# Optimization experiments

Measured on AMD Instinct MI355X. Metric: run time of the kernel, lower is better.

## Reference

```python
import jax, jax.numpy as jnp
import numpy as np
from jax import lax

EPS_LN = 1e-5
EPS_NORM = 1e-12
NUM_HEADS = 8
KV_HEADS = 2
REP = NUM_HEADS // KV_HEADS


def _layernorm_c(x, w, b):
    # WithBias LayerNorm over channel dim; x: [b,c,h,w]
    mu = x.mean(axis=1, keepdims=True)
    var = ((x - mu) ** 2).mean(axis=1, keepdims=True)
    return (x - mu) / jnp.sqrt(var + EPS_LN) * w[None, :, None, None] + b[None, :, None, None]


def _conv1x1(x, w):
    # x: [b,c,h,w], w: [o,c]
    return jnp.einsum('bchw,oc->bohw', x, w)


def _dwconv3x3(x, w):
    # depthwise 3x3, SAME padding; w: [C,1,3,3]
    C = x.shape[1]
    return lax.conv_general_dilated(
        x, w, window_strides=(1, 1), padding='SAME',
        dimension_numbers=('NCHW', 'OIHW', 'NCHW'), feature_group_count=C)


def _l2norm(x):
    # normalize over last axis (torch F.normalize semantics)
    n = jnp.sqrt(jnp.sum(x * x, axis=-1, keepdims=True))
    return x / jnp.maximum(n, EPS_NORM)


def setup_inputs() -> dict:
    key = jax.random.key(0)
    ks = jax.random.split(key, 8)
    b, dim, h, w = 4, 192, 256, 256
    kv_ch = 2 * dim // REP  # 96
    return {
        'x': jax.random.normal(ks[0], (b, dim, h, w), jnp.float32),
        'ln_w': jnp.ones((dim,), jnp.float32),
        'ln_b': jnp.zeros((dim,), jnp.float32),
        'q_w': jax.random.normal(ks[1], (dim, dim), jnp.float32) * 0.02,
        'q_dw': jax.random.normal(ks[2], (dim, 1, 3, 3), jnp.float32) * 0.1,
        'kv_w': jax.random.normal(ks[3], (kv_ch, dim), jnp.float32) * 0.02,
        'kv_dw': jax.random.normal(ks[4], (kv_ch, 1, 3, 3), jnp.float32) * 0.1,
        'proj_w': jax.random.normal(ks[5], (dim, dim), jnp.float32) * 0.02,
        'temperature': jnp.ones((NUM_HEADS, 1, 1), jnp.float32),
    }


def reference(x, ln_w, ln_b, q_w, q_dw, kv_w, kv_dw, proj_w, temperature):
    b, c, h, w = x.shape
    xn = _layernorm_c(x, ln_w, ln_b)
    q = _dwconv3x3(_conv1x1(xn, q_w), q_dw)            # [b, c, h, w]
    kv = _dwconv3x3(_conv1x1(xn, kv_w), kv_dw)         # [b, 2c/rep, h, w]
    k, v = jnp.split(kv, 2, axis=1)
    hw = h * w
    ch = c // NUM_HEADS
    q = q.reshape(b, NUM_HEADS, ch, hw)
    k = k.reshape(b, KV_HEADS, ch, hw)
    v = v.reshape(b, KV_HEADS, ch, hw)
    k = jnp.repeat(k, REP, axis=1)                     # repeat_kv
    v = jnp.repeat(v, REP, axis=1)
    q = _l2norm(q)
    k = _l2norm(k)
    attn = jnp.einsum('bhcn,bhdn->bhcd', q, k) * temperature[None]
    attn = jax.nn.softmax(attn, axis=-1)
    out = jnp.einsum('bhcd,bhdn->bhcn', attn, v)
    out = out.reshape(b, c, h, w)
    return _conv1x1(out, proj_w)
```

## Files before the change

kernel.cpp:

```cpp
#include <hip/hip_runtime.h>
#include <hip/hip_bf16.h>
#include <stdint.h>

#define HW    65536
#define NB    4
#define CIN   192
#define OYC   288
#define BSTR  200
#define EPS2  264

__device__ __forceinline__ float bflo(unsigned u){ return __uint_as_float(u << 16); }
__device__ __forceinline__ float bfhi(unsigned u){ return __uint_as_float(u & 0xffff0000u); }
__device__ __forceinline__ float bf2f(__hip_bfloat16 v){ return __bfloat162float(v); }
__device__ __forceinline__ unsigned short f2bfbits(float f){
  __hip_bfloat16 h = __float2bfloat16(f); return *(unsigned short*)&h;
}

__device__ __forceinline__ void unpack8(uint4 u, float* f) {
  f[0]=bflo(u.x); f[1]=bfhi(u.x); f[2]=bflo(u.y); f[3]=bfhi(u.y);
  f[4]=bflo(u.z); f[5]=bfhi(u.z); f[6]=bflo(u.w); f[7]=bfhi(u.w);
}

union BF8 { uint4 u; __hip_bfloat16 h[8]; };

typedef __attribute__((ext_vector_type(8))) short short8;
typedef __attribute__((ext_vector_type(4))) float floatx4;

__global__ void k_prep(const float* __restrict__ qw, const float* __restrict__ kvw,
                       const float* __restrict__ lnw, const float* __restrict__ lnb,
                       __hip_bfloat16* __restrict__ AF, float* __restrict__ bias,
                       float* __restrict__ Ssum) {
  int blk = blockIdx.x, t = threadIdx.x;
  if (blk < 32) {
    for (int i = blk * 256 + t; i < OYC * CIN; i += 32 * 256) {
      int o = i / CIN, c = i % CIN;
      float w = (o < 192) ? qw[o * 192 + c] : kvw[(o - 192) * 192 + c];
      float val = w * lnw[c];
      int ot = o >> 4, lo = o & 15;
      int ks = c >> 5, cr = c & 31, q = cr >> 3, j = cr & 7;
      int dst = (((ot * 6 + ks) * 64) + q * 16 + lo) * 8 + j;
      AF[dst] = __float2bfloat16(val);
    }
  } else {
    for (int o = t; o < OYC; o += 256) {
      float s = 0.f, s2 = 0.f;
      for (int c = 0; c < CIN; ++c) {
        float w = (o < 192) ? qw[o * 192 + c] : kvw[(o - 192) * 192 + c];
        s += w * lnb[c];
        s2 += bf2f(__float2bfloat16(w * lnw[c]));
      }
      bias[o] = s;
      Ssum[o] = s2;
    }
  }
}

__global__ __launch_bounds__(512, 2) void k_conv1r(const float* __restrict__ x,
                                                   const __hip_bfloat16* __restrict__ AF,
                                                   const float* __restrict__ bias,
                                                   const float* __restrict__ Ssum,
                                                   __hip_bfloat16* __restrict__ y) {
  __shared__ __align__(16) __hip_bfloat16 Bl[256 * BSTR];
  __shared__ float part_s[8][256];
  __shared__ float part_q[8][256];
  __shared__ float murs[256][2];
  __shared__ float biasl[OYC];
  __shared__ float Sl[OYC];

  int bid = blockIdx.x;
  int b = bid >> 8;
  int r = bid & 255;
  int tid = threadIdx.x;
  int w = tid >> 6, l = tid & 63;

  for (int i = tid; i < OYC; i += 512) { biasl[i] = bias[i]; Sl[i] = Ssum[i]; }

  {
    const float* xb = x + (size_t)(b * CIN + w * 24) * HW + r * 256 + l * 4;
    float s[4] = {0.f, 0.f, 0.f, 0.f}, q2[4] = {0.f, 0.f, 0.f, 0.f};
    unsigned pk[4][12];
#pragma unroll
    for (int c = 0; c < 24; ++c) {
      float4 v4 = *(const float4*)(xb + (size_t)c * HW);
      float vv[4] = {v4.x, v4.y, v4.z, v4.w};
#pragma unroll
      for (int i = 0; i < 4; ++i) {
        s[i] += vv[i]; q2[i] += vv[i] * vv[i];
        unsigned bits = f2bfbits(vv[i]);
        if ((c & 1) == 0) pk[i][c >> 1] = bits;
        else              pk[i][c >> 1] |= bits << 16;
      }
    }
#pragma unroll
    for (int i = 0; i < 4; ++i) {
      int px = l * 4 + i;
#pragma unroll
      for (int j = 0; j < 3; ++j) {
        uint4 u = make_uint4(pk[i][j*4], pk[i][j*4+1], pk[i][j*4+2], pk[i][j*4+3]);
        *(uint4*)&Bl[px * BSTR + w * 24 + j * 8] = u;
      }
    }
    *(float4*)&part_s[w][l * 4] = make_float4(s[0], s[1], s[2], s[3]);
    *(float4*)&part_q[w][l * 4] = make_float4(q2[0], q2[1], q2[2], q2[3]);
  }
  __syncthreads();

  int lane = tid & 63;
  int mh = w >> 2, nq = w & 3;
  int li = lane & 15, qd = lane >> 4;

  floatx4 acc[9][4];
#pragma unroll
  for (int t = 0; t < 9; ++t)
#pragma unroll
    for (int nt = 0; nt < 4; ++nt) acc[t][nt] = (floatx4){0.f, 0.f, 0.f, 0.f};

  const __hip_bfloat16* abase = AF + ((size_t)(mh * 9) * 6 * 64 + lane) * 8;
  short8 a0[9], a1[9];
#pragma unroll
  for (int t = 0; t < 9; ++t) a0[t] = *(const short8*)(abase + (size_t)(t * 6) * 512);

#pragma unroll
  for (int ks = 0; ks < 6; ++ks) {
    short8 bf[4];
#pragma unroll
    for (int nt = 0; nt < 4; ++nt) {
      int px = nq * 64 + nt * 16 + li;
      bf[nt] = *(const short8*)&Bl[px * BSTR + ks * 32 + qd * 8];
    }
    if (ks < 5) {
#pragma unroll
      for (int t = 0; t < 9; ++t) {
        short8 v = *(const short8*)(abase + (size_t)(t * 6 + ks + 1) * 512);
        if (ks & 1) a0[t] = v; else a1[t] = v;
      }
    }
#pragma unroll
    for (int t = 0; t < 9; ++t) {
      short8 af = (ks & 1) ? a1[t] : a0[t];
#pragma unroll
      for (int nt = 0; nt < 4; ++nt)
        acc[t][nt] = __builtin_amdgcn_mfma_f32_16x16x32_bf16(af, bf[nt], acc[t][nt], 0, 0, 0);
    }
  }

  if (tid < 256) {
    float s0 = 0.f, s1 = 0.f;
#pragma unroll
    for (int g = 0; g < 8; ++g) { s0 += part_s[g][tid]; s1 += part_q[g][tid]; }
    float m = s0 * (1.f / CIN);
    float var = s1 * (1.f / CIN) - m * m;
    murs[tid][0] = m;
    murs[tid][1] = rsqrtf(var + 1e-5f);
  }

  __hip_bfloat16* EP = Bl;
#pragma unroll
  for (int ph = 0; ph < 2; ++ph) {
    __syncthreads();
    if (mh == ph) {
#pragma unroll
      for (int t = 0; t < 9; ++t)
#pragma unroll
        for (int nt = 0; nt < 4; ++nt) {
          int px = nq * 64 + nt * 16 + li;
          float mu = murs[px][0], rs = murs[px][1];
#pragma unroll
          for (int rr = 0; rr < 4; ++rr) {
            int ol = t * 16 + qd * 4 + rr;
            float val = rs * (acc[t][nt][rr] - mu * Sl[ph * 144 + ol]) + biasl[ph * 144 + ol];
            EP[ol * EPS2 + px] = __float2bfloat16(val);
          }
        }
    }
    __syncthreads();
    for (int i = tid; i < 144 * 32; i += 512) {
      int row = i >> 5, seg = i & 31;
      uint4 u = *(const uint4*)&EP[row * EPS2 + seg * 8];
      *(uint4*)&y[(size_t)(b * OYC + ph * 144 + row) * HW + r * 256 + seg * 8] = u;
    }
  }
}

__global__ __launch_bounds__(256) void k_dwkv(const __hip_bfloat16* __restrict__ y,
                                              const float* __restrict__ kvdw,
                                              __hip_bfloat16* __restrict__ kbuf,
                                              __hip_bfloat16* __restrict__ vbuf,
                                              float* __restrict__ kss) {
  __shared__ __align__(16) __hip_bfloat16 stage[18 * 256];
  int bid = blockIdx.x;
  int hb = bid & 15;
  int ck = (bid >> 4) % 96;
  int b  = bid / (16 * 96);
  int tid = threadIdx.x;
  int h0 = hb * 16;

  const __hip_bfloat16* yp = y + (size_t)(b * OYC + 192 + ck) * HW;
  for (int i = tid; i < 18 * 32; i += 256) {
    int ry = i >> 5, seg = i & 31;
    int hh = h0 - 1 + ry;
    uint4 u = make_uint4(0u, 0u, 0u, 0u);
    if ((unsigned)hh < 256u) u = *(const uint4*)(yp + hh * 256 + seg * 8);
    *(uint4*)&stage[ry * 256 + seg * 8] = u;
  }
  __syncthreads();

  float w[9];
#pragma unroll
  for (int i = 0; i < 9; ++i) w[i] = kvdw[ck * 9 + i];

  int cg = tid & 31, rg = tid >> 5;
  int c0 = cg * 8;
  bool isk = (ck < 48);
  __hip_bfloat16* ob = (isk ? kbuf : vbuf) + (size_t)(b * 48 + (ck % 48)) * HW;
  float ssq = 0.f;
#pragma unroll
  for (int rr = 0; rr < 2; ++rr) {
    int orow = rg * 2 + rr;
    float o[8];
#pragma unroll
    for (int j = 0; j < 8; ++j) o[j] = 0.f;
#pragma unroll
    for (int ry = 0; ry < 3; ++ry) {
      const __hip_bfloat16* rb = &stage[(orow + ry) * 256];
      float v[8];
      unpack8(*(const uint4*)&rb[c0], v);
      float vl = (c0 > 0)       ? bf2f(rb[c0 - 1]) : 0.f;
      float vr = (c0 + 8 < 256) ? bf2f(rb[c0 + 8]) : 0.f;
      float wl = w[ry * 3], wm = w[ry * 3 + 1], wr = w[ry * 3 + 2];
      o[0] = fmaf(wl, vl, fmaf(wm, v[0], fmaf(wr, v[1], o[0])));
#pragma unroll
      for (int j = 1; j < 7; ++j)
        o[j] = fmaf(wl, v[j-1], fmaf(wm, v[j], fmaf(wr, v[j+1], o[j])));
      o[7] = fmaf(wl, v[6], fmaf(wm, v[7], fmaf(wr, vr, o[7])));
    }
    BF8 t;
#pragma unroll
    for (int j = 0; j < 8; ++j) {
      t.h[j] = __float2bfloat16(o[j]);
      if (isk) { float fv = bf2f(t.h[j]); ssq += fv * fv; }
    }
    *(uint4*)(ob + (size_t)(h0 + orow) * 256 + c0) = t.u;
  }
  if (isk) {
#pragma unroll
    for (int off = 32; off > 0; off >>= 1) ssq += __shfl_down(ssq, off);
    __shared__ float ws4[4];
    if ((tid & 63) == 0) ws4[tid >> 6] = ssq;
    __syncthreads();
    if (tid == 0) atomicAdd(&kss[b * 48 + ck], ws4[0] + ws4[1] + ws4[2] + ws4[3]);
  }
}

__global__ __launch_bounds__(256) void k_dwq(const __hip_bfloat16* __restrict__ y,
                                             const float* __restrict__ qdw,
                                             __hip_bfloat16* __restrict__ qfull,
                                             float* __restrict__ qss) {
  __shared__ __align__(16) __hip_bfloat16 stage[18 * 256];
  int bid = blockIdx.x;
  int hb = bid & 15;
  int c  = (bid >> 4) % 192;
  int b  = bid / (16 * 192);
  int tid = threadIdx.x;
  int h0 = hb * 16;

  const __hip_bfloat16* yp = y + (size_t)(b * OYC + c) * HW;
  for (int i = tid; i < 18 * 32; i += 256) {
    int ry = i >> 5, seg = i & 31;
    int hh = h0 - 1 + ry;
    uint4 u = make_uint4(0u, 0u, 0u, 0u);
    if ((unsigned)hh < 256u) u = *(const uint4*)(yp + hh * 256 + seg * 8);
    *(uint4*)&stage[ry * 256 + seg * 8] = u;
  }
  __syncthreads();

  float w[9];
#pragma unroll
  for (int i = 0; i < 9; ++i) w[i] = qdw[c * 9 + i];

  int cg = tid & 31, rg = tid >> 5;
  int c0 = cg * 8;
  __hip_bfloat16* ob = qfull + (size_t)(b * CIN + c) * HW;
  float ssq = 0.f;
#pragma unroll
  for (int rr = 0; rr < 2; ++rr) {
    int orow = rg * 2 + rr;
    float o[8];
#pragma unroll
    for (int j = 0; j < 8; ++j) o[j] = 0.f;
#pragma unroll
    for (int ry = 0; ry < 3; ++ry) {
      const __hip_bfloat16* rb = &stage[(orow + ry) * 256];
      float v[8];
      unpack8(*(const uint4*)&rb[c0], v);
      float vl = (c0 > 0)       ? bf2f(rb[c0 - 1]) : 0.f;
      float vr = (c0 + 8 < 256) ? bf2f(rb[c0 + 8]) : 0.f;
      float wl = w[ry * 3], wm = w[ry * 3 + 1], wr = w[ry * 3 + 2];
      o[0] = fmaf(wl, vl, fmaf(wm, v[0], fmaf(wr, v[1], o[0])));
#pragma unroll
      for (int j = 1; j < 7; ++j)
        o[j] = fmaf(wl, v[j-1], fmaf(wm, v[j], fmaf(wr, v[j+1], o[j])));
      o[7] = fmaf(wl, v[6], fmaf(wm, v[7], fmaf(wr, vr, o[7])));
    }
    BF8 t;
#pragma unroll
    for (int j = 0; j < 8; ++j) {
      t.h[j] = __float2bfloat16(o[j]);
      float fv = bf2f(t.h[j]); ssq += fv * fv;
    }
    *(uint4*)(ob + (size_t)(h0 + orow) * 256 + c0) = t.u;
  }
#pragma unroll
  for (int off = 32; off > 0; off >>= 1) ssq += __shfl_down(ssq, off);
  __shared__ float ws4[4];
  if ((tid & 63) == 0) ws4[tid >> 6] = ssq;
  __syncthreads();
  if (tid == 0) atomicAdd(&qss[b * 192 + c], ws4[0] + ws4[1] + ws4[2] + ws4[3]);
}

__global__ __launch_bounds__(256) void k_qk(const __hip_bfloat16* __restrict__ qfull,
                                            const __hip_bfloat16* __restrict__ kbuf,
                                            float* __restrict__ attn) {
  __shared__ __align__(16) __hip_bfloat16 ql[96 * 264];
  __shared__ __align__(16) __hip_bfloat16 kl[24 * 264];
  __shared__ float red[96 * 33];
  int bid = blockIdx.x;
  int ck  = bid & 63;
  int kvh = (bid >> 6) & 1;
  int b   = bid >> 7;
  int tid = threadIdx.x;
  int wave = tid >> 6, lane = tid & 63;
  int li = lane & 15, qd = lane >> 4;

  for (int i = tid; i < 96 * 33; i += 256) red[i] = 0.f;

  const __hip_bfloat16* qp = qfull + (size_t)(b * CIN + kvh * 96) * HW + ck * 1024;
  const __hip_bfloat16* kp = kbuf  + (size_t)(b * 48 + kvh * 24) * HW + ck * 1024;

  floatx4 acc[6][2];
#pragma unroll
  for (int mt = 0; mt < 6; ++mt) {
    acc[mt][0] = (floatx4){0.f, 0.f, 0.f, 0.f};
    acc[mt][1] = (floatx4){0.f, 0.f, 0.f, 0.f};
  }

  int kr1 = 16 + li; if (kr1 > 23) kr1 = 23;
  for (int sc = 0; sc < 4; ++sc) {
    __syncthreads();
    for (int i = tid; i < 96 * 32; i += 256) {
      int row = i >> 5, seg = i & 31;
      *(uint4*)&ql[row * 264 + seg * 8] = *(const uint4*)(qp + (size_t)row * HW + sc * 256 + seg * 8);
    }
    for (int i = tid; i < 24 * 32; i += 256) {
      int row = i >> 5, seg = i & 31;
      *(uint4*)&kl[row * 264 + seg * 8] = *(const uint4*)(kp + (size_t)row * HW + sc * 256 + seg * 8);
    }
    __syncthreads();
#pragma unroll
    for (int ks = 0; ks < 2; ++ks) {
      int off = wave * 64 + ks * 32 + qd * 8;
      short8 bk0 = *(const short8*)&kl[li  * 264 + off];
      short8 bk1 = *(const short8*)&kl[kr1 * 264 + off];
#pragma unroll
      for (int mt = 0; mt < 6; ++mt) {
        short8 aq = *(const short8*)&ql[(mt * 16 + li) * 264 + off];
        acc[mt][0] = __builtin_amdgcn_mfma_f32_16x16x32_bf16(aq, bk0, acc[mt][0], 0, 0, 0);
        acc[mt][1] = __builtin_amdgcn_mfma_f32_16x16x32_bf16(aq, bk1, acc[mt][1], 0, 0, 0);
      }
    }
  }

#pragma unroll
  for (int mt = 0; mt < 6; ++mt) {
#pragma unroll
    for (int nt = 0; nt < 2; ++nt) {
      int n = nt * 16 + li;
      if (n < 24) {
#pragma unroll
        for (int r = 0; r < 4; ++r) {
          int m = mt * 16 + qd * 4 + r;
          atomicAdd(&red[m * 33 + n], acc[mt][nt][r]);
        }
      }
    }
  }
  __syncthreads();

  for (int i = tid; i < 96 * 24; i += 256) {
    int m = i / 24, d = i % 24;
    int head = kvh * 4 + m / 24, cp = m % 24;
    atomicAdd(&attn[(((b * 8 + head) * 24) + cp) * 24 + d], red[m * 33 + d]);
  }
}

__global__ void k_attn_final(const float* __restrict__ attn, const float* __restrict__ qss,
                             const float* __restrict__ kss, const float* __restrict__ temp,
                             const float* __restrict__ projw, __hip_bfloat16* __restrict__ AB) {
  int b = blockIdx.x;
  int t = threadIdx.x;
  __shared__ float as_[96 * 25];
  float acc[48];
#pragma unroll
  for (int j = 0; j < 48; ++j) acc[j] = 0.f;
  for (int kvh = 0; kvh < 2; ++kvh) {
    __syncthreads();
    if (t < 96) {
      int row = kvh * 96 + t;
      int h = row / 24, cp = row % 24;
      float rq = 1.f / fmaxf(sqrtf(qss[b * 192 + row]), 1e-12f);
      float tp = temp[h];
      float lg[24]; float mx = -1e30f;
#pragma unroll
      for (int d = 0; d < 24; ++d) {
        float rk = 1.f / fmaxf(sqrtf(kss[b * 48 + kvh * 24 + d]), 1e-12f);
        float l = attn[(((b * 8 + h) * 24) + cp) * 24 + d] * rq * rk * tp;
        lg[d] = l; mx = fmaxf(mx, l);
      }
      float s = 0.f;
#pragma unroll
      for (int d = 0; d < 24; ++d) { lg[d] = __expf(lg[d] - mx); s += lg[d]; }
      float inv = 1.f / s;
#pragma unroll
      for (int d = 0; d < 24; ++d) as_[t * 25 + d] = lg[d] * inv;
    }
    __syncthreads();
    if (t < 192) {
      for (int cc = 0; cc < 96; ++cc) {
        float pw = projw[t * 192 + kvh * 96 + cc];
        const float* ar = &as_[cc * 25];
#pragma unroll
        for (int d = 0; d < 24; ++d) acc[kvh * 24 + d] = fmaf(pw, ar[d], acc[kvh * 24 + d]);
      }
    }
  }
  if (t < 192) {
    __hip_bfloat16* ABb = AB + (size_t)b * 18432;
    int mt = t >> 4, lb = t & 15;
#pragma unroll
    for (int g = 0; g < 12; ++g) {
      int kk0 = g * 8;
      int s = kk0 >> 5;
      int lane = lb + 16 * ((kk0 & 31) >> 3);
      BF8 u;
#pragma unroll
      for (int jj = 0; jj < 8; ++jj) {
        int kk = kk0 + jj;
        if (kk < 48) {
          u.h[jj] = __float2bfloat16(acc[kk]);
        } else {
          int j = kk - 48;
          float hv = bf2f(__float2bfloat16(acc[j]));
          u.h[jj] = __float2bfloat16(acc[j] - hv);
        }
      }
      *(uint4*)(ABb + (size_t)((mt * 3 + s) * 64 + lane) * 8) = u.u;
    }
  }
}

__global__ __launch_bounds__(512) void k_out(const __hip_bfloat16* __restrict__ vbuf,
                                             const __hip_bfloat16* __restrict__ AB,
                                             float* __restrict__ out) {
  __shared__ __align__(16) __hip_bfloat16 vT[256 * 56];
  __shared__ __align__(16) float EPu[48 * 260];
  __hip_bfloat16* vl = (__hip_bfloat16*)EPu;

  int bid = blockIdx.x;
  int b  = bid >> 8;
  int n0 = (bid & 255) * 256;
  int tid = threadIdx.x;

  const __hip_bfloat16* vb = vbuf + (size_t)b * 48 * HW + n0;
  for (int i = tid; i < 48 * 32; i += 512) {
    int j = i >> 5, seg = i & 31;
    *(uint4*)&vl[j * 264 + seg * 8] = *(const uint4*)(vb + (size_t)j * HW + seg * 8);
  }
  __syncthreads();
  for (int i = tid; i < 256 * 6; i += 512) {
    int px = i & 255, j0 = (i >> 8) * 8;
    BF8 u;
#pragma unroll
    for (int e = 0; e < 8; ++e) u.h[e] = vl[(j0 + e) * 264 + px];
    *(uint4*)&vT[px * 56 + j0] = u.u;
  }
  __syncthreads();

  int w = tid >> 6, lane = tid & 63;
  int li = lane & 15, qd = lane >> 4;
  int mg = w & 3;
  int nh = w >> 2;

  const __hip_bfloat16* ABb = AB + (size_t)b * 18432;

  floatx4 acc[3][8];
#pragma unroll
  for (int m = 0; m < 3; ++m)
#pragma unroll
    for (int nt = 0; nt < 8; ++nt) acc[m][nt] = (floatx4){0.f, 0.f, 0.f, 0.f};

#pragma unroll
  for (int s = 0; s < 3; ++s) {
    short8 a[3];
#pragma unroll
    for (int m = 0; m < 3; ++m)
      a[m] = *(const short8*)(ABb + (size_t)(((mg * 3 + m) * 3 + s) * 64 + lane) * 8);
    int t0 = s * 32 + qd * 8;
    int j0 = (t0 >= 48) ? t0 - 48 : t0;
#pragma unroll
    for (int nt = 0; nt < 8; ++nt) {
      int n = nh * 128 + nt * 16 + li;
      short8 bv = *(const short8*)&vT[n * 56 + j0];
#pragma unroll
      for (int m = 0; m < 3; ++m)
        acc[m][nt] = __builtin_amdgcn_mfma_f32_16x16x32_bf16(a[m], bv, acc[m][nt], 0, 0, 0);
    }
  }

#pragma unroll
  for (int ph = 0; ph < 4; ++ph) {
    __syncthreads();
    if (mg == ph) {
#pragma unroll
      for (int m = 0; m < 3; ++m)
#pragma unroll
        for (int nt = 0; nt < 8; ++nt) {
          int col = nh * 128 + nt * 16 + li;
#pragma unroll
          for (int r = 0; r < 4; ++r)
            EPu[(m * 16 + qd * 4 + r) * 260 + col] = acc[m][nt][r];
        }
    }
    __syncthreads();
    for (int i = tid; i < 48 * 64; i += 512) {
      int row = i >> 6, c4 = (i & 63) * 4;
      float4 v4 = *(const float4*)&EPu[row * 260 + c4];
      *(float4*)&out[(size_t)(b * 192 + ph * 48 + row) * HW + n0 + c4] = v4;
    }
  }
}

extern "C" void kernel_launch(void* const* d_in, const int* in_sizes, int n_in,
                              void* d_out, int out_size, void* d_ws, size_t ws_size,
                              hipStream_t stream) {
  const float* x     = (const float*)d_in[0];
  const float* ln_w  = (const float*)d_in[1];
  const float* ln_b  = (const float*)d_in[2];
  const float* q_w   = (const float*)d_in[3];
  const float* q_dw  = (const float*)d_in[4];
  const float* kv_w  = (const float*)d_in[5];
  const float* kv_dw = (const float*)d_in[6];
  const float* projw = (const float*)d_in[7];
  const float* temp  = (const float*)d_in[8];
  float* out = (float*)d_out;
  float* wsf = (float*)d_ws;

  float* qss  = wsf;
  float* kss  = wsf + 768;
  float* attn = wsf + 960;
  __hip_bfloat16* AB = (__hip_bfloat16*)(wsf + 19392);
  float* bias = wsf + 56256;
  float* Ssum = wsf + 56544;
  __hip_bfloat16* AF = (__hip_bfloat16*)(wsf + 56832);
  __hip_bfloat16* y    = (__hip_bfloat16*)(wsf + 111872);
  __hip_bfloat16* kbuf = (__hip_bfloat16*)(wsf + 37860608);
  __hip_bfloat16* vbuf = (__hip_bfloat16*)(wsf + 44152064);
  __hip_bfloat16* qfull = (__hip_bfloat16*)d_out;

  hipMemsetAsync(wsf, 0, 19392 * sizeof(float), stream);
  hipLaunchKernelGGL(k_prep, dim3(33), dim3(256), 0, stream, q_w, kv_w, ln_w, ln_b, AF, bias, Ssum);
  hipLaunchKernelGGL(k_conv1r, dim3(NB * 256), dim3(512), 0, stream, x, AF, bias, Ssum, y);
  hipLaunchKernelGGL(k_dwkv, dim3(NB * 96 * 16), dim3(256), 0, stream, y, kv_dw, kbuf, vbuf, kss);
  hipLaunchKernelGGL(k_dwq,  dim3(NB * 192 * 16), dim3(256), 0, stream, y, q_dw, qfull, qss);
  hipLaunchKernelGGL(k_qk,   dim3(NB * 2 * 64), dim3(256), 0, stream, qfull, kbuf, attn);
  hipLaunchKernelGGL(k_attn_final, dim3(NB), dim3(256), 0, stream, attn, qss, kss, temp, projw, AB);
  hipLaunchKernelGGL(k_out,  dim3(NB * 256), dim3(512), 0, stream, vbuf, AB, out);
}
```

Baseline: 607.6 us.

## Fuse depthwise q conv into QK^T kernel, avoiding full q materialization

Merges the depthwise 3x3 conv for q with the q·k^T MFMA reduction. Each block stages a 6-row halo of 32 y channels in shared memory and computes q rows on the fly into LDS. It then multiplies them against k rows, so the full bf16 q tensor is never written to or read from global memory. The cost is redundant halo loads (6 rows loaded per 4 output rows), more syncs per block, and more shared-memory atomics for the q sum-of-squares.

```diff
diff --git a/kernel.cpp b/kernel.cpp
--- a/kernel.cpp
+++ b/kernel.cpp
@@ -252,126 +252,102 @@
   }
 }
 
-__global__ __launch_bounds__(256) void k_dwq(const __hip_bfloat16* __restrict__ y,
-                                             const float* __restrict__ qdw,
-                                             __hip_bfloat16* __restrict__ qfull,
-                                             float* __restrict__ qss) {
-  __shared__ __align__(16) __hip_bfloat16 stage[18 * 256];
-  int bid = blockIdx.x;
-  int hb = bid & 15;
-  int c  = (bid >> 4) % 192;
-  int b  = bid / (16 * 192);
+__global__ __launch_bounds__(512) void k_dwqk(const __hip_bfloat16* __restrict__ y,
+                                              const float* __restrict__ qdw,
+                                              const __hip_bfloat16* __restrict__ kbuf,
+                                              float* __restrict__ qss,
+                                              float* __restrict__ attn) {
+  __shared__ __align__(16) __hip_bfloat16 ys[32 * 6 * 256];
+  __shared__ __align__(16) __hip_bfloat16 ql[32 * 264];
+  __shared__ __align__(16) __hip_bfloat16 kl[24 * 264];
+  __shared__ float red[32 * 33];
+  __shared__ float qssl[32];
+
+  int t = blockIdx.x;
+  int band = t & 63; t >>= 6;
+  int qh = t % 3; t /= 3;
+  int kvh = t & 1;
+  int b = t >> 1;
   int tid = threadIdx.x;
-  int h0 = hb * 16;
-
-  const __hip_bfloat16* yp = y + (size_t)(b * OYC + c) * HW;
-  for (int i = tid; i < 18 * 32; i += 256) {
-    int ry = i >> 5, seg = i & 31;
-    int hh = h0 - 1 + ry;
+  int r0 = band * 4;
+  int chg0 = kvh * 96 + qh * 32;
+
+  for (int i = tid; i < 32 * 33; i += 512) red[i] = 0.f;
+  if (tid < 32) qssl[tid] = 0.f;
+
+  for (int i = tid; i < 6144; i += 512) {
+    int ch = i / 192, rem = i % 192;
+    int ry = rem >> 5, seg = rem & 31;
+    int hh = r0 - 1 + ry;
     uint4 u = make_uint4(0u, 0u, 0u, 0u);
-    if ((unsigned)hh < 256u) u = *(const uint4*)(yp + hh * 256 + seg * 8);
-    *(uint4*)&stage[ry * 256 + seg * 8] = u;
-  }
-  __syncthreads();
-
-  float w[9];
-#pragma unroll
-  for (int i = 0; i < 9; ++i) w[i] = qdw[c * 9 + i];
-
-  int cg = tid & 31, rg = tid >> 5;
-  int c0 = cg * 8;
-  __hip_bfloat16* ob = qfull + (size_t)(b * CIN + c) * HW;
-  float ssq = 0.f;
-#pragma unroll
-  for (int rr = 0; rr < 2; ++rr) {
-    int orow = rg * 2 + rr;
-    float o[8];
-#pragma unroll
-    for (int j = 0; j < 8; ++j) o[j] = 0.f;
-#pragma unroll
-    for (int ry = 0; ry < 3; ++ry) {
-      const __hip_bfloat16* rb = &stage[(orow + ry) * 256];
-      float v[8];
-      unpack8(*(const uint4*)&rb[c0], v);
-      float vl = (c0 > 0)       ? bf2f(rb[c0 - 1]) : 0.f;
-      float vr = (c0 + 8 < 256) ? bf2f(rb[c0 + 8]) : 0.f;
-      float wl = w[ry * 3], wm = w[ry * 3 + 1], wr = w[ry * 3 + 2];
-      o[0] = fmaf(wl, vl, fmaf(wm, v[0], fmaf(wr, v[1], o[0])));
-#pragma unroll
-      for (int j = 1; j < 7; ++j)
-        o[j] = fmaf(wl, v[j-1], fmaf(wm, v[j], fmaf(wr, v[j+1], o[j])));
-      o[7] = fmaf(wl, v[6], fmaf(wm, v[7], fmaf(wr, vr, o[7])));
-    }
-    BF8 t;
-#pragma unroll
-    for (int j = 0; j < 8; ++j) {
-      t.h[j] = __float2bfloat16(o[j]);
-      float fv = bf2f(t.h[j]); ssq += fv * fv;
-    }
-    *(uint4*)(ob + (size_t)(h0 + orow) * 256 + c0) = t.u;
-  }
-#pragma unroll
-  for (int off = 32; off > 0; off >>= 1) ssq += __shfl_down(ssq, off);
-  __shared__ float ws4[4];
-  if ((tid & 63) == 0) ws4[tid >> 6] = ssq;
-  __syncthreads();
-  if (tid == 0) atomicAdd(&qss[b * 192 + c], ws4[0] + ws4[1] + ws4[2] + ws4[3]);
-}
-
-__global__ __launch_bounds__(256) void k_qk(const __hip_bfloat16* __restrict__ qfull,
-                                            const __hip_bfloat16* __restrict__ kbuf,
-                                            float* __restrict__ attn) {
-  __shared__ __align__(16) __hip_bfloat16 ql[96 * 264];
-  __shared__ __align__(16) __hip_bfloat16 kl[24 * 264];
-  __shared__ float red[96 * 33];
-  int bid = blockIdx.x;
-  int ck  = bid & 63;
-  int kvh = (bid >> 6) & 1;
-  int b   = bid >> 7;
-  int tid = threadIdx.x;
-  int wave = tid >> 6, lane = tid & 63;
+    if ((unsigned)hh < 256u)
+      u = *(const uint4*)(y + (size_t)(b * OYC + chg0 + ch) * HW + hh * 256 + seg * 8);
+    *(uint4*)&ys[(ch * 6 + ry) * 256 + seg * 8] = u;
+  }
+  __syncthreads();
+
+  int wv = tid >> 6, lane = tid & 63;
   int li = lane & 15, qd = lane >> 4;
-
-  for (int i = tid; i < 96 * 33; i += 256) red[i] = 0.f;
-
-  const __hip_bfloat16* qp = qfull + (size_t)(b * CIN + kvh * 96) * HW + ck * 1024;
-  const __hip_bfloat16* kp = kbuf  + (size_t)(b * 48 + kvh * 24) * HW + ck * 1024;
-
-  floatx4 acc[6][2];
-#pragma unroll
-  for (int mt = 0; mt < 6; ++mt) {
-    acc[mt][0] = (floatx4){0.f, 0.f, 0.f, 0.f};
-    acc[mt][1] = (floatx4){0.f, 0.f, 0.f, 0.f};
-  }
-
   int kr1 = 16 + li; if (kr1 > 23) kr1 = 23;
-  for (int sc = 0; sc < 4; ++sc) {
-    __syncthreads();
-    for (int i = tid; i < 96 * 32; i += 256) {
-      int row = i >> 5, seg = i & 31;
-      *(uint4*)&ql[row * 264 + seg * 8] = *(const uint4*)(qp + (size_t)row * HW + sc * 256 + seg * 8);
-    }
-    for (int i = tid; i < 24 * 32; i += 256) {
-      int row = i >> 5, seg = i & 31;
-      *(uint4*)&kl[row * 264 + seg * 8] = *(const uint4*)(kp + (size_t)row * HW + sc * 256 + seg * 8);
-    }
-    __syncthreads();
-#pragma unroll
-    for (int ks = 0; ks < 2; ++ks) {
-      int off = wave * 64 + ks * 32 + qd * 8;
+
+  floatx4 acc[2][2];
+  acc[0][0] = (floatx4){0.f,0.f,0.f,0.f}; acc[0][1] = (floatx4){0.f,0.f,0.f,0.f};
+  acc[1][0] = (floatx4){0.f,0.f,0.f,0.f}; acc[1][1] = (floatx4){0.f,0.f,0.f,0.f};
+
+  const __hip_bfloat16* kp = kbuf + (size_t)(b * 48 + kvh * 24) * HW;
+
+  for (int rr = 0; rr < 4; ++rr) {
+    if (rr) __syncthreads();
+    for (int i = tid; i < 1024; i += 512) {
+      int ch = i >> 5, seg = i & 31, c0 = seg * 8;
+      const float* wp = qdw + (chg0 + ch) * 9;
+      float o[8];
+#pragma unroll
+      for (int j = 0; j < 8; ++j) o[j] = 0.f;
+#pragma unroll
+      for (int ry = 0; ry < 3; ++ry) {
+        const __hip_bfloat16* rb = &ys[(ch * 6 + rr + ry) * 256];
+        float v[8];
+        unpack8(*(const uint4*)&rb[c0], v);
+        float vl = (c0 > 0)       ? bf2f(rb[c0 - 1]) : 0.f;
+        float vr = (c0 + 8 < 256) ? bf2f(rb[c0 + 8]) : 0.f;
+        float wl = wp[ry * 3], wm = wp[ry * 3 + 1], wr = wp[ry * 3 + 2];
+        o[0] = fmaf(wl, vl, fmaf(wm, v[0], fmaf(wr, v[1], o[0])));
+#pragma unroll
+        for (int j = 1; j < 7; ++j)
+          o[j] = fmaf(wl, v[j-1], fmaf(wm, v[j], fmaf(wr, v[j+1], o[j])));
+        o[7] = fmaf(wl, v[6], fmaf(wm, v[7], fmaf(wr, vr, o[7])));
+      }
+      BF8 u; float part = 0.f;
+#pragma unroll
+      for (int j = 0; j < 8; ++j) {
+        u.h[j] = __float2bfloat16(o[j]);
+        float fv = bf2f(u.h[j]); part += fv * fv;
+      }
+      *(uint4*)&ql[ch * 264 + c0] = u.u;
+      atomicAdd(&qssl[ch], part);
+    }
+    for (int i = tid; i < 768; i += 512) {
+      int ch = i >> 5, seg = i & 31;
+      *(uint4*)&kl[ch * 264 + seg * 8] =
+        *(const uint4*)(kp + (size_t)ch * HW + (r0 + rr) * 256 + seg * 8);
+    }
+    __syncthreads();
+    {
+      int off = wv * 32 + qd * 8;
       short8 bk0 = *(const short8*)&kl[li  * 264 + off];
       short8 bk1 = *(const short8*)&kl[kr1 * 264 + off];
 #pragma unroll
-      for (int mt = 0; mt < 6; ++mt) {
+      for (int mt = 0; mt < 2; ++mt) {
         short8 aq = *(const short8*)&ql[(mt * 16 + li) * 264 + off];
         acc[mt][0] = __builtin_amdgcn_mfma_f32_16x16x32_bf16(aq, bk0, acc[mt][0], 0, 0, 0);
         acc[mt][1] = __builtin_amdgcn_mfma_f32_16x16x32_bf16(aq, bk1, acc[mt][1], 0, 0, 0);
       }
     }
   }
-
-#pragma unroll
-  for (int mt = 0; mt < 6; ++mt) {
+  __syncthreads();
+#pragma unroll
+  for (int mt = 0; mt < 2; ++mt) {
 #pragma unroll
     for (int nt = 0; nt < 2; ++nt) {
       int n = nt * 16 + li;
@@ -385,12 +361,13 @@
     }
   }
   __syncthreads();
-
-  for (int i = tid; i < 96 * 24; i += 256) {
+  for (int i = tid; i < 32 * 24; i += 512) {
     int m = i / 24, d = i % 24;
-    int head = kvh * 4 + m / 24, cp = m % 24;
+    int cc = qh * 32 + m;
+    int head = kvh * 4 + cc / 24, cp = cc % 24;
     atomicAdd(&attn[(((b * 8 + head) * 24) + cp) * 24 + d], red[m * 33 + d]);
   }
+  if (tid < 32) atomicAdd(&qss[b * 192 + chg0 + tid], qssl[tid]);
 }
 
 __global__ void k_attn_final(const float* __restrict__ attn, const float* __restrict__ qss,
@@ -564,14 +541,12 @@
   __hip_bfloat16* y    = (__hip_bfloat16*)(wsf + 111872);
   __hip_bfloat16* kbuf = (__hip_bfloat16*)(wsf + 37860608);
   __hip_bfloat16* vbuf = (__hip_bfloat16*)(wsf + 44152064);
-  __hip_bfloat16* qfull = (__hip_bfloat16*)d_out;
 
   hipMemsetAsync(wsf, 0, 19392 * sizeof(float), stream);
   hipLaunchKernelGGL(k_prep, dim3(33), dim3(256), 0, stream, q_w, kv_w, ln_w, ln_b, AF, bias, Ssum);
   hipLaunchKernelGGL(k_conv1r, dim3(NB * 256), dim3(512), 0, stream, x, AF, bias, Ssum, y);
   hipLaunchKernelGGL(k_dwkv, dim3(NB * 96 * 16), dim3(256), 0, stream, y, kv_dw, kbuf, vbuf, kss);
-  hipLaunchKernelGGL(k_dwq,  dim3(NB * 192 * 16), dim3(256), 0, stream, y, q_dw, qfull, qss);
-  hipLaunchKernelGGL(k_qk,   dim3(NB * 2 * 64), dim3(256), 0, stream, qfull, kbuf, attn);
+  hipLaunchKernelGGL(k_dwqk, dim3(NB * 2 * 3 * 64), dim3(512), 0, stream, y, q_dw, kbuf, qss, attn);
   hipLaunchKernelGGL(k_attn_final, dim3(NB), dim3(256), 0, stream, attn, qss, kss, temp, projw, AB);
-  hipLaunchKernelGGL(k_out,  dim3(NB * 256), dim3(512), 0, stream, vbuf, AB, out);
-}
+  hipLaunchKernelGGL(k_out, dim3(NB * 256), dim3(512), 0, stream, vbuf, AB, out);
+}
```

New measurement: 667.0 us. 9.8% more time.
